# Kernel optimization log

Measured on AMD Instinct MI355X. Metric: run time of the kernel, lower is better.

## Reference

```python
import jax, jax.numpy as jnp
import numpy as np

EMBED_DIM = 1024
Q_HEADS = 8
KV_HEADS = 4
HEAD_DIM = EMBED_DIM // Q_HEADS          # 128
KV_EMBED_DIM = HEAD_DIM * KV_HEADS       # 512
LN_EPS = 1e-5
RMS_EPS = 1e-6


def _activation_quant(x):
    # per-token int8 quant over last dim
    scale = 127.0 / jnp.clip(jnp.max(jnp.abs(x), axis=-1, keepdims=True), 1e-5)
    return jnp.clip(jnp.round(x * scale), -128, 127) / scale


def _weight_quant(w):
    # ternary (sign) quant with global mean-abs scale
    scale = jnp.mean(jnp.abs(w))
    e = jnp.mean(w)
    return jnp.sign(w - e) * scale


def bit_linear(x, w):
    # fresh RMSNorm with weight=ones (as in the torch code: RMSNorm(d)(x))
    x_norm = x * jax.lax.rsqrt(jnp.mean(x * x, axis=-1, keepdims=True) + RMS_EPS)
    # straight-through estimators
    x_q = x_norm + jax.lax.stop_gradient(_activation_quant(x_norm) - x_norm)
    w_q = w + jax.lax.stop_gradient(_weight_quant(w) - w)
    # F.linear(x_quant, w_quant): NO bias (the torch forward ignores self.bias)
    return jnp.einsum('bnd,od->bno', x_q, w_q)


def setup_inputs() -> dict:
    key = jax.random.key(0)
    ks = jax.random.split(key, 7)
    B, S = 4, 2048

    def xavier(k, shape):
        std = (2.0 / (shape[0] + shape[1])) ** 0.5
        return std * jax.random.normal(k, shape, dtype=jnp.float32)

    return {
        'query': jax.random.normal(ks[0], (B, S, EMBED_DIM), dtype=jnp.float32),
        'key':   jax.random.normal(ks[1], (B, S, EMBED_DIM), dtype=jnp.float32),
        'value': jax.random.normal(ks[2], (B, S, EMBED_DIM), dtype=jnp.float32),
        'q_w':   xavier(ks[3], (EMBED_DIM, EMBED_DIM)),
        'k_w':   xavier(ks[4], (KV_EMBED_DIM, EMBED_DIM)),
        'v_w':   xavier(ks[5], (KV_EMBED_DIM, EMBED_DIM)),
        'out_w': xavier(ks[6], (EMBED_DIM, KV_EMBED_DIM)),
        'ln_gamma': jnp.ones((KV_EMBED_DIM,), dtype=jnp.float32),
        'ln_beta':  jnp.zeros((KV_EMBED_DIM,), dtype=jnp.float32),
    }


def reference(query, key, value, q_w, k_w, v_w, out_w, ln_gamma, ln_beta):
    B, N, _ = query.shape
    q = bit_linear(query, q_w)   # [b, n, embed_dim]
    k = bit_linear(key,   k_w)   # [b, s, kv_embed_dim]
    v = bit_linear(value, v_w)   # [b, s, kv_embed_dim]

    g = Q_HEADS // KV_HEADS  # head groups
    # b n (hq d) -> b hq n d -> b hk g n d  (head index = h*g + g_idx, matching
    # einops 'b (h g) n d -> b g h n d')
    q = q.reshape(B, N, Q_HEADS, HEAD_DIM).transpose(0, 2, 1, 3)
    q = q.reshape(B, KV_HEADS, g, N, HEAD_DIM)
    k = k.reshape(B, -1, KV_HEADS, HEAD_DIM).transpose(0, 2, 1, 3)  # b h s d
    v = v.reshape(B, -1, KV_HEADS, HEAD_DIM).transpose(0, 2, 1, 3)  # b h s d

    scale = HEAD_DIM ** 0.5
    q = q / scale
    # note: the original SUMS over the group axis g (faithful to einops einsum)
    sim = jnp.einsum('bhgnd,bhsd->bhns', q, k)
    # note: original divides by scale AGAIN before softmax
    attn = jax.nn.softmax(sim / scale, axis=-1)
    out = jnp.einsum('bhns,bhsd->bnhd', attn, v)        # b n hk d
    x = out.reshape(B, N, KV_EMBED_DIM)

    # LayerNorm over kv_embed_dim
    mu = jnp.mean(x, axis=-1, keepdims=True)
    var = jnp.mean((x - mu) ** 2, axis=-1, keepdims=True)
    x = (x - mu) * jax.lax.rsqrt(var + LN_EPS) * ln_gamma + ln_beta

    return bit_linear(x, out_w)  # [b, n, embed_dim]
```

## Files before the change

kernel.cpp:

```cpp
#include <hip/hip_runtime.h>
#include <cstdint>
#include <cstddef>

constexpr int B_   = 4;
constexpr int SEQ  = 2048;
constexpr int E    = 1024;
constexpr int KVE  = 512;
constexpr int H    = 4;
constexpr int ROWS = B_ * SEQ;
constexpr int NSPLIT = 2;
constexpr int KVT  = SEQ / NSPLIT;
constexpr int NT   = KVT / 64;

typedef short short8   __attribute__((ext_vector_type(8)));
typedef short short4v  __attribute__((ext_vector_type(4)));
typedef float floatx4  __attribute__((ext_vector_type(4)));
typedef float floatx16 __attribute__((ext_vector_type(16)));
typedef int   intx4    __attribute__((ext_vector_type(4)));

__device__ inline short f2bf(float f) {
    uint32_t u = __builtin_bit_cast(uint32_t, f);
    u = (u + 0x7fff + ((u >> 16) & 1)) >> 16;
    return (short)u;
}
__device__ inline float bf2f(short s) {
    return __builtin_bit_cast(float, (uint32_t)(uint16_t)s << 16);
}
__device__ inline void gl_lds16(const void* g, void* l) {
    __builtin_amdgcn_global_load_lds(
        (const __attribute__((address_space(1))) unsigned int*)g,
        (__attribute__((address_space(3))) unsigned int*)l, 16, 0, 0);
}

__global__ __launch_bounds__(256) void pre_kernel(
    const float* __restrict__ qx, const float* __restrict__ kx,
    const float* __restrict__ vx,
    const float* __restrict__ w0, const float* __restrict__ w1,
    const float* __restrict__ w2, const float* __restrict__ w3,
    int8_t* __restrict__ xq01, int8_t* __restrict__ xq2,
    float* __restrict__ dqv, float* __restrict__ stats)
{
    int tid = threadIdx.x, bid = blockIdx.x;
    int lane = tid & 63, wv = tid >> 6;
    if (bid < 256) {
        int m = bid >> 6;
        const float* w = (m == 0) ? w0 : (m == 1) ? w1 : (m == 2) ? w2 : w3;
        int n4 = ((m == 0) ? 1024 * 1024 : 512 * 1024) >> 2;
        float s = 0.f, sa = 0.f;
        for (int i = (bid & 63) * 256 + tid; i < n4; i += 64 * 256) {
            float4 x = ((const float4*)w)[i];
            s += x.x + x.y + x.z + x.w;
            sa += fabsf(x.x) + fabsf(x.y) + fabsf(x.z) + fabsf(x.w);
        }
#pragma unroll
        for (int o = 32; o; o >>= 1) { s += __shfl_xor(s, o); sa += __shfl_xor(sa, o); }
        __shared__ float ls[4], lsa[4];
        if (!lane) { ls[wv] = s; lsa[wv] = sa; }
        __syncthreads();
        if (!tid) {
            atomicAdd(&stats[2 * m],     ls[0] + ls[1] + ls[2] + ls[3]);
            atomicAdd(&stats[2 * m + 1], lsa[0] + lsa[1] + lsa[2] + lsa[3]);
        }
        return;
    }
    int rowi = (bid - 256) * 4 + wv;
    int z = rowi >> 13, r = rowi & (ROWS - 1);
    const float* x = (z == 0) ? qx : (z == 1) ? kx : vx;
    int8_t* xq = (z == 2) ? xq2 : xq01 + (size_t)z * ROWS * E;
    size_t base = (size_t)r * E;
    float4 v[4];
    float ss = 0.f, am = 0.f;
#pragma unroll
    for (int j = 0; j < 4; j++) {
        v[j] = *(const float4*)(x + base + lane * 4 + j * 256);
        ss += v[j].x * v[j].x + v[j].y * v[j].y + v[j].z * v[j].z + v[j].w * v[j].w;
        am = fmaxf(am, fmaxf(fmaxf(fabsf(v[j].x), fabsf(v[j].y)),
                             fmaxf(fabsf(v[j].z), fabsf(v[j].w))));
    }
#pragma unroll
    for (int o = 32; o; o >>= 1) { ss += __shfl_xor(ss, o); am = fmaxf(am, __shfl_xor(am, o)); }
    float rms = rsqrtf(ss * (1.0f / E) + 1e-6f);
    float cl  = fmaxf(am * rms, 1e-5f);
    float kf  = rms * (127.0f / cl);
#pragma unroll
    for (int j = 0; j < 4; j++) {
        int q0 = max(-128, min(127, (int)rintf(v[j].x * kf)));
        int q1 = max(-128, min(127, (int)rintf(v[j].y * kf)));
        int q2 = max(-128, min(127, (int)rintf(v[j].z * kf)));
        int q3 = max(-128, min(127, (int)rintf(v[j].w * kf)));
        uint32_t pk = (uint32_t)(q0 & 0xff) | ((uint32_t)(q1 & 0xff) << 8) |
                      ((uint32_t)(q2 & 0xff) << 16) | ((uint32_t)(q3 & 0xff) << 24);
        *(uint32_t*)(xq + base + lane * 4 + j * 256) = pk;
    }
    if (!lane) dqv[(size_t)z * ROWS + r] = cl * (1.0f / 127.0f);
}

__global__ __launch_bounds__(256) void wquant_kernel(
    const float* __restrict__ w0, const float* __restrict__ w1,
    const float* __restrict__ w2, const float* __restrict__ w3,
    int n0, int n1, int n2, int n3, const float* __restrict__ stats,
    int8_t* __restrict__ o0, int8_t* __restrict__ o1,
    int8_t* __restrict__ o2, int8_t* __restrict__ o3)
{
    int m = blockIdx.y;
    const float* w = (m == 0) ? w0 : (m == 1) ? w1 : (m == 2) ? w2 : w3;
    int n = (m == 0) ? n0 : (m == 1) ? n1 : (m == 2) ? n2 : n3;
    int8_t* o = (m == 0) ? o0 : (m == 1) ? o1 : (m == 2) ? o2 : o3;
    float e = stats[2 * m] / (float)n;
    int n4 = n >> 2;
    for (int i = blockIdx.x * 256 + threadIdx.x; i < n4; i += gridDim.x * 256) {
        float4 x = ((const float4*)w)[i];
        int q0 = (x.x > e) - (x.x < e);
        int q1 = (x.y > e) - (x.y < e);
        int q2 = (x.z > e) - (x.z < e);
        int q3 = (x.w > e) - (x.w < e);
        uint32_t pk = (uint32_t)(q0 & 0xff) | ((uint32_t)(q1 & 0xff) << 8) |
                      ((uint32_t)(q2 & 0xff) << 16) | ((uint32_t)(q3 & 0xff) << 24);
        *(uint32_t*)(o + ((size_t)i << 2)) = pk;
    }
}

template <bool F32OUT>
__device__ inline void gemm_body(
    const int8_t* __restrict__ A, const int8_t* __restrict__ W,
    const float* __restrict__ dqv, float sw, void* __restrict__ Cout,
    int O, int K, int8_t* As, int8_t* Ws, size_t row0, size_t c0)
{
    int tid = threadIdx.x;
    int w = tid >> 6, lane = tid & 63;
    int quad = lane >> 4, l15 = lane & 15;
    int mbase = (w & 1) * 64, nbase = (w >> 1) * 64;

    intx4 acc[4][4];
#pragma unroll
    for (int i = 0; i < 4; i++)
#pragma unroll
        for (int j = 0; j < 4; j++) acc[i][j] = (intx4){0, 0, 0, 0};

    const int8_t* Ag[4]; const int8_t* Wg[4]; int8_t* lA[4]; int8_t* lW[4];
#pragma unroll
    for (int t = 0; t < 4; t++) {
        int c = tid + t * 256;
        int row = c >> 3, g = (c & 7) ^ (row & 7);
        Ag[t] = A + (row0 + row) * K + g * 16;
        Wg[t] = W + (c0 + row) * K + g * 16;
        lA[t] = As + c * 16;
        lW[t] = Ws + c * 16;
    }

    for (int kt = 0; kt < K; kt += 128) {
        __syncthreads();
#pragma unroll
        for (int t = 0; t < 4; t++) {
            gl_lds16(Ag[t] + kt, lA[t]);
            gl_lds16(Wg[t] + kt, lW[t]);
        }
        __syncthreads();
#pragma unroll
        for (int kh = 0; kh < 2; kh++) {
            intx4 af[4], bfr[4];
#pragma unroll
            for (int mt = 0; mt < 4; mt++) {
                int row = mbase + mt * 16 + l15;
                int pos = (quad + 4 * kh) ^ (row & 7);
                af[mt] = *(const intx4*)(As + row * 128 + pos * 16);
            }
#pragma unroll
            for (int nt = 0; nt < 4; nt++) {
                int row = nbase + nt * 16 + l15;
                int pos = (quad + 4 * kh) ^ (row & 7);
                bfr[nt] = *(const intx4*)(Ws + row * 128 + pos * 16);
            }
#pragma unroll
            for (int mt = 0; mt < 4; mt++)
#pragma unroll
                for (int nt = 0; nt < 4; nt++)
                    acc[mt][nt] = __builtin_amdgcn_mfma_i32_16x16x64_i8(
                        af[mt], bfr[nt], acc[mt][nt], 0, 0, 0);
        }
    }

#pragma unroll
    for (int mt = 0; mt < 4; mt++) {
#pragma unroll
        for (int r = 0; r < 4; r++) {
            size_t grow = row0 + mbase + mt * 16 + quad * 4 + r;
            float scv = sw * dqv[grow];
#pragma unroll
            for (int nt = 0; nt < 4; nt++) {
                size_t gcol = c0 + nbase + nt * 16 + l15;
                float v = (float)acc[mt][nt][r] * scv;
                if constexpr (F32OUT) ((float*)Cout)[grow * O + gcol] = v;
                else                  ((short*)Cout)[grow * O + gcol] = f2bf(v);
            }
        }
    }
}

__global__ __launch_bounds__(256) void gemm_qkv(
    const int8_t* __restrict__ xq01, const int8_t* __restrict__ xq2,
    const int8_t* __restrict__ wq_q, const int8_t* __restrict__ wq_k,
    const int8_t* __restrict__ wq_v, const float* __restrict__ dqv,
    const float* __restrict__ stats,
    short* __restrict__ qb, short* __restrict__ kb, short* __restrict__ vb)
{
    __shared__ int8_t As[128 * 128];
    __shared__ int8_t Ws[128 * 128];
    int id = blockIdx.x;
    int z, bx, by;
    if (id < 512)      { z = 0; bx = id & 7; by = id >> 3; }
    else if (id < 768) { z = 1; int t = id - 512; bx = t & 3; by = t >> 2; }
    else               { z = 2; int t = id - 768; bx = t & 3; by = t >> 2; }
    int O = z ? KVE : E;
    const int8_t* A = (z == 0) ? xq01 : (z == 1) ? xq01 + (size_t)ROWS * E : xq2;
    const int8_t* W = (z == 0) ? wq_q : (z == 1) ? wq_k : wq_v;
    short* outp = (z == 0) ? qb : (z == 1) ? kb : vb;
    float sw = stats[2 * z + 1] / (float)(O * E);
    gemm_body<false>(A, W, dqv + (size_t)z * ROWS, sw, outp, O, E, As, Ws,
                     (size_t)by * 128, (size_t)bx * 128);
}

__global__ __launch_bounds__(256) void gemm_out(
    const int8_t* __restrict__ A, const int8_t* __restrict__ W,
    const float* __restrict__ dqv, const float* __restrict__ stats,
    float* __restrict__ Cout)
{
    __shared__ int8_t As[128 * 128];
    __shared__ int8_t Ws[128 * 128];
    float sw = stats[7] / (float)(E * KVE);
    gemm_body<true>(A, W, dqv, sw, Cout, E, KVE, As, Ws,
                    (size_t)blockIdx.y * 128, (size_t)blockIdx.x * 128);
}

__global__ __launch_bounds__(256, 2) void attn_mfma(
    const short* __restrict__ qb, const short* __restrict__ kb,
    const short* __restrict__ vb, short* __restrict__ opart,
    float* __restrict__ mlbuf)
{
    __shared__ short Ks[64][132];
    __shared__ short Vt[128][68];
    int tid = threadIdx.x;
    int w = tid >> 6, lane = tid & 63;
    int l31 = lane & 31, hi = lane >> 5;
    int id = blockIdx.x;
    int b    = id >> 7;
    int q    = (id >> 3) & 15;
    int h    = (id >> 1) & 3;
    int part = id & 1;
    size_t qrow0 = ((size_t)b * 16 + q) * 128;
    size_t sbase = (size_t)b * SEQ + (size_t)part * KVT;

    int sK = tid >> 2, cK = tid & 3;
    int sV = (tid & 15) * 4, dV = tid >> 4;

    short8 kreg[4], vreg[4];
    {
        const short* ksrc = kb + (sbase + sK) * KVE + h * 128 + cK * 32;
#pragma unroll
        for (int j = 0; j < 4; j++) kreg[j] = *(const short8*)(ksrc + j * 8);
        const short* vsrc = vb + (sbase + sV) * KVE + h * 128 + dV * 8;
#pragma unroll
        for (int j = 0; j < 4; j++) vreg[j] = *(const short8*)(vsrc + j * KVE);
    }

    short8 qfrag[8];
    {
        const short* src = qb + (qrow0 + w * 32 + l31) * E + h * 256 + hi * 8;
        constexpr float C = 1.44269504089f * (1.0f / 128.0f);
#pragma unroll
        for (int j = 0; j < 8; j++) {
            short8 a  = *(const short8*)(src + j * 16);
            short8 b2 = *(const short8*)(src + j * 16 + 128);
            short8 o;
#pragma unroll
            for (int e = 0; e < 8; e++)
                o[e] = f2bf((bf2f(a[e]) + bf2f(b2[e])) * C);
            qfrag[j] = o;
        }
    }

    floatx16 oacc[4];
#pragma unroll
    for (int dt = 0; dt < 4; dt++)
#pragma unroll
        for (int r = 0; r < 16; r++) oacc[dt][r] = 0.f;
    float m_s = -1e30f, l_s = 0.f;

    for (int st = 0; st < NT; st++) {
        __syncthreads();
#pragma unroll
        for (int j = 0; j < 4; j++)
            *(short8*)&Ks[sK][cK * 32 + j * 8] = kreg[j];
#pragma unroll
        for (int i = 0; i < 8; i++) {
            short4v vv = { vreg[0][i], vreg[1][i], vreg[2][i], vreg[3][i] };
            *(short4v*)&Vt[dV * 8 + i][sV] = vv;
        }
        if (st + 1 < NT) {
            size_t srow0 = sbase + (size_t)(st + 1) * 64;
            const short* ksrc = kb + (srow0 + sK) * KVE + h * 128 + cK * 32;
#pragma unroll
            for (int j = 0; j < 4; j++) kreg[j] = *(const short8*)(ksrc + j * 8);
            const short* vsrc = vb + (srow0 + sV) * KVE + h * 128 + dV * 8;
#pragma unroll
            for (int j = 0; j < 4; j++) vreg[j] = *(const short8*)(vsrc + j * KVE);
        }
        __syncthreads();
        floatx16 sc0, sc1;
#pragma unroll
        for (int r = 0; r < 16; r++) { sc0[r] = 0.f; sc1[r] = 0.f; }
#pragma unroll
        for (int j = 0; j < 8; j++) {
            short8 kf0 = *(const short8*)&Ks[l31][j * 16 + hi * 8];
            short8 kf1 = *(const short8*)&Ks[32 + l31][j * 16 + hi * 8];
            sc0 = __builtin_amdgcn_mfma_f32_32x32x16_bf16(kf0, qfrag[j], sc0, 0, 0, 0);
            sc1 = __builtin_amdgcn_mfma_f32_32x32x16_bf16(kf1, qfrag[j], sc1, 0, 0, 0);
        }
        float mx = sc0[0];
#pragma unroll
        for (int r = 0; r < 16; r++) mx = fmaxf(mx, fmaxf(sc0[r], sc1[r]));
        mx = fmaxf(mx, __shfl_xor(mx, 32));
        float pm = fmaxf(m_s, mx);
        if (!__all(pm - m_s <= 8.0f)) {
            float alpha = __builtin_amdgcn_exp2f(m_s - pm);
            m_s = pm;
            l_s *= alpha;
#pragma unroll
            for (int dt = 0; dt < 4; dt++)
#pragma unroll
                for (int r = 0; r < 16; r++) oacc[dt][r] *= alpha;
        }
        float rs = 0.f;
#pragma unroll
        for (int r = 0; r < 16; r++) {
            float p0 = __builtin_amdgcn_exp2f(sc0[r] - m_s); sc0[r] = p0; rs += p0;
            float p1 = __builtin_amdgcn_exp2f(sc1[r] - m_s); sc1[r] = p1; rs += p1;
        }
        rs += __shfl_xor(rs, 32);
        l_s += rs;
        uint32_t w0[8], w1[8];
#pragma unroll
        for (int i = 0; i < 8; i++) {
            asm("v_cvt_pk_bf16_f32 %0, %1, %2"
                : "=v"(w0[i]) : "v"(sc0[2 * i]), "v"(sc0[2 * i + 1]));
            asm("v_cvt_pk_bf16_f32 %0, %1, %2"
                : "=v"(w1[i]) : "v"(sc1[2 * i]), "v"(sc1[2 * i + 1]));
        }
#pragma unroll
        for (int i = 0; i < 2; i++) {
            { auto r = __builtin_amdgcn_permlane32_swap(w0[i], w0[i + 2], false, false);
              w0[i] = r[0]; w0[i + 2] = r[1]; }
            { auto r = __builtin_amdgcn_permlane32_swap(w0[i + 4], w0[i + 6], false, false);
              w0[i + 4] = r[0]; w0[i + 6] = r[1]; }
            { auto r = __builtin_amdgcn_permlane32_swap(w1[i], w1[i + 2], false, false);
              w1[i] = r[0]; w1[i + 2] = r[1]; }
            { auto r = __builtin_amdgcn_permlane32_swap(w1[i + 4], w1[i + 6], false, false);
              w1[i + 4] = r[0]; w1[i + 6] = r[1]; }
        }
        short8 pb[4];
        {
            intx4 t0 = { (int)w0[0], (int)w0[1], (int)w0[2], (int)w0[3] };
            intx4 t1 = { (int)w0[4], (int)w0[5], (int)w0[6], (int)w0[7] };
            intx4 t2 = { (int)w1[0], (int)w1[1], (int)w1[2], (int)w1[3] };
            intx4 t3 = { (int)w1[4], (int)w1[5], (int)w1[6], (int)w1[7] };
            pb[0] = __builtin_bit_cast(short8, t0);
            pb[1] = __builtin_bit_cast(short8, t1);
            pb[2] = __builtin_bit_cast(short8, t2);
            pb[3] = __builtin_bit_cast(short8, t3);
        }
#pragma unroll
        for (int dt = 0; dt < 4; dt++)
#pragma unroll
            for (int j = 0; j < 4; j++) {
                short8 vf = *(const short8*)&Vt[dt * 32 + l31][j * 16 + hi * 8];
                oacc[dt] = __builtin_amdgcn_mfma_f32_32x32x16_bf16(vf, pb[j], oacc[dt], 0, 0, 0);
            }
    }
    {
        float inv = 1.0f / l_s;
        size_t grow = qrow0 + w * 32 + l31;
        short* dst = opart + ((size_t)part * ROWS + grow) * KVE + h * 128;
#pragma unroll
        for (int dt = 0; dt < 4; dt++)
#pragma unroll
            for (int c = 0; c < 4; c++) {
                short4v o4 = { f2bf(oacc[dt][c * 4] * inv),
                               f2bf(oacc[dt][c * 4 + 1] * inv),
                               f2bf(oacc[dt][c * 4 + 2] * inv),
                               f2bf(oacc[dt][c * 4 + 3] * inv) };
                *(short4v*)(dst + dt * 32 + c * 8 + hi * 4) = o4;
            }
        if (hi == 0) {
            float* ml = mlbuf + (((size_t)part * ROWS + grow) * H + h) * 2;
            ml[0] = m_s;
            ml[1] = l_s;
        }
    }
}

__global__ __launch_bounds__(256) void ln_combine_kernel(
    const short* __restrict__ opart, const float* __restrict__ mlbuf,
    const float* __restrict__ gamma, const float* __restrict__ beta,
    int8_t* __restrict__ xq, float* __restrict__ dqv)
{
    int lane = threadIdx.x & 63, wv = threadIdx.x >> 6;
    int row = blockIdx.x * 4 + wv;
    float4 y[2];
    float s = 0.f, ss = 0.f;
#pragma unroll
    for (int j = 0; j < 2; j++) {
        int col = lane * 4 + j * 256;
        int h = j * 2 + (lane >> 5);
        float mv[NSPLIT], lv[NSPLIT];
        float M = -1e30f;
#pragma unroll
        for (int p = 0; p < NSPLIT; p++) {
            const float* ml = mlbuf + (((size_t)p * ROWS + row) * H + h) * 2;
            mv[p] = ml[0]; lv[p] = ml[1];
            M = fmaxf(M, mv[p]);
        }
        float wt[NSPLIT], wsum = 0.f;
#pragma unroll
        for (int p = 0; p < NSPLIT; p++) {
            wt[p] = lv[p] * __builtin_amdgcn_exp2f(mv[p] - M);
            wsum += wt[p];
        }
        float winv = 1.0f / wsum;
        float4 vv = { 0.f, 0.f, 0.f, 0.f };
#pragma unroll
        for (int p = 0; p < NSPLIT; p++) {
            short4v o = *(const short4v*)(opart + ((size_t)p * ROWS + row) * KVE + col);
            float wp = wt[p] * winv;
            vv.x += bf2f(o.x) * wp;
            vv.y += bf2f(o.y) * wp;
            vv.z += bf2f(o.z) * wp;
            vv.w += bf2f(o.w) * wp;
        }
        y[j] = vv;
        s += vv.x + vv.y + vv.z + vv.w;
        ss += vv.x * vv.x + vv.y * vv.y + vv.z * vv.z + vv.w * vv.w;
    }
#pragma unroll
    for (int o = 32; o; o >>= 1) { s += __shfl_xor(s, o); ss += __shfl_xor(ss, o); }
    float mu = s * (1.0f / KVE);
    float var = fmaxf(ss * (1.0f / KVE) - mu * mu, 0.0f);
    float inv = rsqrtf(var + 1e-5f);
    float sy = 0.f, am = 0.f;
#pragma unroll
    for (int j = 0; j < 2; j++) {
        int col = lane * 4 + j * 256;
        float4 g = *(const float4*)(gamma + col);
        float4 be = *(const float4*)(beta + col);
        y[j].x = (y[j].x - mu) * inv * g.x + be.x;
        y[j].y = (y[j].y - mu) * inv * g.y + be.y;
        y[j].z = (y[j].z - mu) * inv * g.z + be.z;
        y[j].w = (y[j].w - mu) * inv * g.w + be.w;
        sy += y[j].x * y[j].x + y[j].y * y[j].y + y[j].z * y[j].z + y[j].w * y[j].w;
        am = fmaxf(am, fmaxf(fmaxf(fabsf(y[j].x), fabsf(y[j].y)),
                             fmaxf(fabsf(y[j].z), fabsf(y[j].w))));
    }
#pragma unroll
    for (int o = 32; o; o >>= 1) { sy += __shfl_xor(sy, o); am = fmaxf(am, __shfl_xor(am, o)); }
    float rms = rsqrtf(sy * (1.0f / KVE) + 1e-6f);
    float cl = fmaxf(am * rms, 1e-5f);
    float kf = rms * (127.0f / cl);
#pragma unroll
    for (int j = 0; j < 2; j++) {
        int col = lane * 4 + j * 256;
        int q0 = max(-128, min(127, (int)rintf(y[j].x * kf)));
        int q1 = max(-128, min(127, (int)rintf(y[j].y * kf)));
        int q2 = max(-128, min(127, (int)rintf(y[j].z * kf)));
        int q3 = max(-128, min(127, (int)rintf(y[j].w * kf)));
        uint32_t pk = (uint32_t)(q0 & 0xff) | ((uint32_t)(q1 & 0xff) << 8) |
                      ((uint32_t)(q2 & 0xff) << 16) | ((uint32_t)(q3 & 0xff) << 24);
        *(uint32_t*)(xq + (size_t)row * KVE + col) = pk;
    }
    if (!lane) dqv[row] = cl * (1.0f / 127.0f);
}

extern "C" void kernel_launch(void* const* d_in, const int* in_sizes, int n_in,
                              void* d_out, int out_size, void* d_ws, size_t ws_size,
                              hipStream_t stream)
{
    const float* query = (const float*)d_in[0];
    const float* key   = (const float*)d_in[1];
    const float* value = (const float*)d_in[2];
    const float* q_w   = (const float*)d_in[3];
    const float* k_w   = (const float*)d_in[4];
    const float* v_w   = (const float*)d_in[5];
    const float* out_w = (const float*)d_in[6];
    const float* ln_g  = (const float*)d_in[7];
    const float* ln_b  = (const float*)d_in[8];
    float* out = (float*)d_out;

    char* p = (char*)d_ws;
    float* stats = (float*)p;  p += 256;
    int8_t* wq_q = (int8_t*)p; p += (size_t)1024 * 1024;
    int8_t* wq_k = (int8_t*)p; p += (size_t)512 * 1024;
    int8_t* wq_v = (int8_t*)p; p += (size_t)512 * 1024;
    int8_t* wq_o = (int8_t*)p; p += (size_t)1024 * 512;
    int8_t* xq01 = (int8_t*)p; p += (size_t)2 * ROWS * E;
    float* dqv  = (float*)p;   p += (size_t)3 * ROWS * 4;
    short* qb   = (short*)p;   p += (size_t)ROWS * E * 2;
    short* kb   = (short*)p;   p += (size_t)ROWS * KVE * 2;
    short* vb   = (short*)p;   p += (size_t)ROWS * KVE * 2;
    short* opart = (short*)p;  p += (size_t)NSPLIT * ROWS * KVE * 2;
    float* mlbuf = (float*)p;  p += (size_t)NSPLIT * ROWS * H * 2 * 4;
    int8_t* xq2 = (int8_t*)opart;
    if ((size_t)(p - (char*)d_ws) > ws_size) return;

    dim3 blk(256);
    hipMemsetAsync(stats, 0, 256, stream);
    pre_kernel<<<dim3(256 + 3 * ROWS / 4), blk, 0, stream>>>(query, key, value,
        q_w, k_w, v_w, out_w, xq01, xq2, dqv, stats);
    wquant_kernel<<<dim3(64, 4), blk, 0, stream>>>(q_w, k_w, v_w, out_w,
        1024 * 1024, 512 * 1024, 512 * 1024, 1024 * 512, stats, wq_q, wq_k, wq_v, wq_o);

    gemm_qkv<<<dim3(1024), blk, 0, stream>>>(xq01, xq2, wq_q, wq_k, wq_v,
        dqv, stats, qb, kb, vb);

    attn_mfma<<<dim3(512), blk, 0, stream>>>(qb, kb, vb, opart, mlbuf);

    ln_combine_kernel<<<dim3(ROWS / 4), blk, 0, stream>>>(opart, mlbuf,
        ln_g, ln_b, xq01, dqv);
    gemm_out<<<dim3(8, 64), blk, 0, stream>>>(xq01, wq_o, dqv, stats, out);
}
```

Before: 263.0 us.

## Fold query group-sum into Q weights to halve Q projection GEMM

Because attention sums the two grouped query heads before the dot product, the two ternary weight row blocks for each group are pre-added in the weight quant kernel, giving a 512-wide Q weight with values in {-2..2}. The Q GEMM then produces a 512-wide output with the softmax scale folded into its dequant factor, and attention loads Q fragments directly without the add-and-scale pass. This drops a quarter of the QKV GEMM work, halves the Q buffer traffic, and adds a small extra weight-quant pass. The result now comes from an exact int32 accumulation followed by one bf16 rounding, where before two bf16-rounded heads were summed, so numerics shift slightly.

```diff
diff --git a/kernel.cpp b/kernel.cpp
--- a/kernel.cpp
+++ b/kernel.cpp
@@ -100,9 +100,30 @@
     const float* __restrict__ w2, const float* __restrict__ w3,
     int n0, int n1, int n2, int n3, const float* __restrict__ stats,
     int8_t* __restrict__ o0, int8_t* __restrict__ o1,
-    int8_t* __restrict__ o2, int8_t* __restrict__ o3)
+    int8_t* __restrict__ o2, int8_t* __restrict__ o3,
+    int8_t* __restrict__ oqs)
 {
     int m = blockIdx.y;
+    if (m == 4) {
+        float e = stats[0] / (float)(1024 * 1024);
+        int n4 = (512 * 1024) >> 2;
+        for (int i = blockIdx.x * 256 + threadIdx.x; i < n4; i += gridDim.x * 256) {
+            int o = i >> 8;
+            int k4 = i & 255;
+            int r1 = ((o >> 7) * 256 + (o & 127));
+            int b1 = r1 * 256 + k4, b2 = b1 + 128 * 256;
+            float4 x1 = ((const float4*)w0)[b1];
+            float4 x2 = ((const float4*)w0)[b2];
+            int q0 = ((x1.x > e) - (x1.x < e)) + ((x2.x > e) - (x2.x < e));
+            int q1 = ((x1.y > e) - (x1.y < e)) + ((x2.y > e) - (x2.y < e));
+            int q2 = ((x1.z > e) - (x1.z < e)) + ((x2.z > e) - (x2.z < e));
+            int q3 = ((x1.w > e) - (x1.w < e)) + ((x2.w > e) - (x2.w < e));
+            uint32_t pk = (uint32_t)(q0 & 0xff) | ((uint32_t)(q1 & 0xff) << 8) |
+                          ((uint32_t)(q2 & 0xff) << 16) | ((uint32_t)(q3 & 0xff) << 24);
+            *(uint32_t*)(oqs + ((size_t)i << 2)) = pk;
+        }
+        return;
+    }
     const float* w = (m == 0) ? w0 : (m == 1) ? w1 : (m == 2) ? w2 : w3;
     int n = (m == 0) ? n0 : (m == 1) ? n1 : (m == 2) ? n2 : n3;
     int8_t* o = (m == 0) ? o0 : (m == 1) ? o1 : (m == 2) ? o2 : o3;
@@ -199,24 +220,24 @@
 
 __global__ __launch_bounds__(256) void gemm_qkv(
     const int8_t* __restrict__ xq01, const int8_t* __restrict__ xq2,
-    const int8_t* __restrict__ wq_q, const int8_t* __restrict__ wq_k,
+    const int8_t* __restrict__ wq_qs, const int8_t* __restrict__ wq_k,
     const int8_t* __restrict__ wq_v, const float* __restrict__ dqv,
     const float* __restrict__ stats,
-    short* __restrict__ qb, short* __restrict__ kb, short* __restrict__ vb)
+    short* __restrict__ qs, short* __restrict__ kb, short* __restrict__ vb)
 {
     __shared__ int8_t As[128 * 128];
     __shared__ int8_t Ws[128 * 128];
     int id = blockIdx.x;
-    int z, bx, by;
-    if (id < 512)      { z = 0; bx = id & 7; by = id >> 3; }
-    else if (id < 768) { z = 1; int t = id - 512; bx = t & 3; by = t >> 2; }
-    else               { z = 2; int t = id - 768; bx = t & 3; by = t >> 2; }
-    int O = z ? KVE : E;
+    int z = id >> 8;
+    int t = id & 255;
+    int bx = t & 3, by = t >> 2;
     const int8_t* A = (z == 0) ? xq01 : (z == 1) ? xq01 + (size_t)ROWS * E : xq2;
-    const int8_t* W = (z == 0) ? wq_q : (z == 1) ? wq_k : wq_v;
-    short* outp = (z == 0) ? qb : (z == 1) ? kb : vb;
-    float sw = stats[2 * z + 1] / (float)(O * E);
-    gemm_body<false>(A, W, dqv + (size_t)z * ROWS, sw, outp, O, E, As, Ws,
+    const int8_t* W = (z == 0) ? wq_qs : (z == 1) ? wq_k : wq_v;
+    short* outp = (z == 0) ? qs : (z == 1) ? kb : vb;
+    float sw = (z == 0)
+        ? stats[1] / (float)(E * E) * (1.44269504089f / 128.0f)
+        : stats[2 * z + 1] / (float)(KVE * E);
+    gemm_body<false>(A, W, dqv + (size_t)z * ROWS, sw, outp, KVE, E, As, Ws,
                      (size_t)by * 128, (size_t)bx * 128);
 }
 
@@ -233,7 +254,7 @@
 }
 
 __global__ __launch_bounds__(256, 2) void attn_mfma(
-    const short* __restrict__ qb, const short* __restrict__ kb,
+    const short* __restrict__ qs, const short* __restrict__ kb,
     const short* __restrict__ vb, short* __restrict__ opart,
     float* __restrict__ mlbuf)
 {
@@ -265,18 +286,9 @@
 
     short8 qfrag[8];
     {
-        const short* src = qb + (qrow0 + w * 32 + l31) * E + h * 256 + hi * 8;
-        constexpr float C = 1.44269504089f * (1.0f / 128.0f);
-#pragma unroll
-        for (int j = 0; j < 8; j++) {
-            short8 a  = *(const short8*)(src + j * 16);
-            short8 b2 = *(const short8*)(src + j * 16 + 128);
-            short8 o;
-#pragma unroll
-            for (int e = 0; e < 8; e++)
-                o[e] = f2bf((bf2f(a[e]) + bf2f(b2[e])) * C);
-            qfrag[j] = o;
-        }
+        const short* src = qs + (qrow0 + w * 32 + l31) * KVE + h * 128 + hi * 8;
+#pragma unroll
+        for (int j = 0; j < 8; j++) qfrag[j] = *(const short8*)(src + j * 16);
     }
 
     floatx16 oacc[4];
@@ -499,9 +511,10 @@
     int8_t* wq_k = (int8_t*)p; p += (size_t)512 * 1024;
     int8_t* wq_v = (int8_t*)p; p += (size_t)512 * 1024;
     int8_t* wq_o = (int8_t*)p; p += (size_t)1024 * 512;
+    int8_t* wq_qs = (int8_t*)p; p += (size_t)512 * 1024;
     int8_t* xq01 = (int8_t*)p; p += (size_t)2 * ROWS * E;
     float* dqv  = (float*)p;   p += (size_t)3 * ROWS * 4;
-    short* qb   = (short*)p;   p += (size_t)ROWS * E * 2;
+    short* qs   = (short*)p;   p += (size_t)ROWS * KVE * 2;
     short* kb   = (short*)p;   p += (size_t)ROWS * KVE * 2;
     short* vb   = (short*)p;   p += (size_t)ROWS * KVE * 2;
     short* opart = (short*)p;  p += (size_t)NSPLIT * ROWS * KVE * 2;
@@ -513,13 +526,14 @@
     hipMemsetAsync(stats, 0, 256, stream);
     pre_kernel<<<dim3(256 + 3 * ROWS / 4), blk, 0, stream>>>(query, key, value,
         q_w, k_w, v_w, out_w, xq01, xq2, dqv, stats);
-    wquant_kernel<<<dim3(64, 4), blk, 0, stream>>>(q_w, k_w, v_w, out_w,
-        1024 * 1024, 512 * 1024, 512 * 1024, 1024 * 512, stats, wq_q, wq_k, wq_v, wq_o);
-
-    gemm_qkv<<<dim3(1024), blk, 0, stream>>>(xq01, xq2, wq_q, wq_k, wq_v,
-        dqv, stats, qb, kb, vb);
-
-    attn_mfma<<<dim3(512), blk, 0, stream>>>(qb, kb, vb, opart, mlbuf);
+    wquant_kernel<<<dim3(64, 5), blk, 0, stream>>>(q_w, k_w, v_w, out_w,
+        1024 * 1024, 512 * 1024, 512 * 1024, 1024 * 512, stats,
+        wq_q, wq_k, wq_v, wq_o, wq_qs);
+
+    gemm_qkv<<<dim3(768), blk, 0, stream>>>(xq01, xq2, wq_qs, wq_k, wq_v,
+        dqv, stats, qs, kb, vb);
+
+    attn_mfma<<<dim3(512), blk, 0, stream>>>(qs, kb, vb, opart, mlbuf);
 
     ln_combine_kernel<<<dim3(ROWS / 4), blk, 0, stream>>>(opart, mlbuf,
         ln_g, ln_b, xq01, dqv);
```

Result: faster. 248.7 us (-5.4%).
